# Kernel optimization log

Hardware: AMD Instinct MI355X
Metric: run time of the kernel (lower is better)

## Reference

```python
import jax, jax.numpy as jnp
import numpy as np

N, C_IN, C_OUT, T, V = 256, 64, 64, 64, 25
REL = C_IN // 8  # rel_channels = in_channels // rel_reduction (in_channels != 3)


def setup_inputs() -> dict:
    key = jax.random.key(0)
    ks = jax.random.split(key, 10)
    s_in = 1.0 / np.sqrt(C_IN)
    s_rel = 1.0 / np.sqrt(REL)
    return {
        "x": jax.random.normal(ks[0], (N, C_IN, T, V), dtype=jnp.float32),
        "A": jax.random.normal(ks[1], (V, V), dtype=jnp.float32),
        "w1": jax.random.normal(ks[2], (REL, C_IN), dtype=jnp.float32) * s_in,
        "b1": jnp.zeros((REL,), dtype=jnp.float32),
        "w2": jax.random.normal(ks[3], (REL, C_IN), dtype=jnp.float32) * s_in,
        "b2": jnp.zeros((REL,), dtype=jnp.float32),
        "w3": jax.random.normal(ks[4], (C_OUT, REL), dtype=jnp.float32) * s_rel,
        "b3": jnp.zeros((C_OUT,), dtype=jnp.float32),
        "wr": jax.random.normal(ks[5], (C_OUT, C_IN), dtype=jnp.float32) * s_in,
        "br": jnp.zeros((C_OUT,), dtype=jnp.float32),
    }


def reference(x, A, w1, b1, w2, b2, w3, b3, wr, br):
    alpha = 1.0
    # residual: 1x1 conv over channels -> (N, C_OUT, T, V)
    inputs = jnp.einsum('oi,nitv->notv', wr, x) + br[None, :, None, None]
    # conv1/conv2 then temporal mean -> (N, REL, V)
    x1 = jnp.einsum('ri,nitv->nrv', w1, x) / T + b1[None, :, None]
    x2 = jnp.einsum('ri,nitv->nrv', w2, x) / T + b2[None, :, None]
    # broadcast outer difference -> (N, REL, V, V)
    d = jnp.tanh(x1[:, :, :, None] - x2[:, :, None, :])
    # conv3 (1x1 over rel channels) -> (N, C_OUT, V, V); add static A
    Adyn = jnp.einsum('or,nruv->nouv', w3, d) + b3[None, :, None, None]
    Afull = Adyn * alpha + A[None, None, :, :]
    # per-channel batched graph conv: (N,C,V,V) x (N,C,T,V) -> (N,C,T,V)
    out = jnp.einsum('ncuv,nctv->nctu', Afull, inputs)
    return out
```

## Files before the change

### kernel.cpp

```cpp
#include <hip/hip_runtime.h>
#include <cmath>

namespace {
constexpr int NB  = 256;
constexpr int CI  = 64;
constexpr int CO  = 64;
constexpr int TT  = 64;
constexpr int V   = 25;
constexpr int REL = 8;
constexpr int TV  = TT * V;
constexpr int CC  = 8;
constexpr int IP  = 28;
constexpr int AP  = 28;
}

typedef float f4 __attribute__((ext_vector_type(4)));

__device__ __forceinline__ float fast_tanh(float x) {
  float ax = fabsf(x);
  float e  = __expf(-2.f * ax);
  float r  = (1.f - e) / (1.f + e);
  return copysignf(r, x);
}

__global__ __launch_bounds__(1024) void k1_x12(
    const float* __restrict__ x,
    const float* __restrict__ w1, const float* __restrict__ b1,
    const float* __restrict__ w2, const float* __restrict__ b2,
    float* __restrict__ ws) {
  const int n = blockIdx.x;
  const int tid = threadIdx.x;
  __shared__ __align__(16) float xs[8][TV];
  __shared__ float xsum[CI][V];
  __shared__ float w12[2][REL][CI];

  for (int idx = tid; idx < 2 * REL * CI; idx += 1024) {
    int half = idx / (REL * CI), rem = idx % (REL * CI);
    w12[half][rem / CI][rem % CI] = half ? w2[rem] : w1[rem];
  }

  const float4* xb = reinterpret_cast<const float4*>(x + (size_t)n * (CI * TV));
  float4* xsv = reinterpret_cast<float4*>(&xs[0][0]);
  constexpr int V4G = 8 * TV / 4;

  for (int g = 0; g < 8; ++g) {
    __syncthreads();
    for (int idx = tid; idx < V4G; idx += 1024)
      xsv[idx] = xb[g * V4G + idx];
    __syncthreads();
    if (tid < 8 * V) {
      int ch = tid / V, v = tid % V;
      float acc = 0.f;
      #pragma unroll
      for (int t = 0; t < TT; ++t) acc += xs[ch][t * V + v];
      xsum[g * 8 + ch][v] = acc;
    }
  }
  __syncthreads();

  if (tid < 2 * REL * V) {
    int half = tid / (REL * V), rem = tid % (REL * V);
    int r = rem / V, v = rem % V;
    float a = 0.f;
    #pragma unroll
    for (int i = 0; i < CI; ++i) a = fmaf(w12[half][r][i], xsum[i][v], a);
    ws[(size_t)n * (2 * REL * V) + tid] = a * (1.f / TT) + (half ? b2[r] : b1[r]);
  }
}

__global__ __launch_bounds__(512, 4) void k2_fused(
    const float* __restrict__ x, const float* __restrict__ A,
    const float* __restrict__ w3, const float* __restrict__ b3,
    const float* __restrict__ wr, const float* __restrict__ br,
    const float* __restrict__ ws, float* __restrict__ out) {
  const int id  = blockIdx.x;
  const int n   = (id & 7) | ((id >> 3) & ~7);
  const int cb  = (id >> 3) & 7;
  const int c0  = cb * CC;
  const int tid = threadIdx.x;

  __shared__ __align__(16) float inp[CC * TT * IP];
  __shared__ __align__(16) float Afs[CC * V * AP];

  {
    float* row = inp + tid * IP;
    row[25] = 0.f; row[26] = 0.f; row[27] = 0.f;
  }

  const float* x1n = ws + (size_t)n * (2 * REL * V);
  const float* x2n = x1n + REL * V;
  for (int idx = tid; idx < V * AP; idx += 512) {
    int u = idx / AP, v = idx % AP;
    if (v < V) {
      float t8[REL];
      #pragma unroll
      for (int r = 0; r < REL; ++r)
        t8[r] = fast_tanh(x1n[r * V + u] - x2n[r * V + v]);
      const float base = A[u * V + v];
      #pragma unroll
      for (int cc = 0; cc < CC; ++cc) {
        float acc = base + b3[c0 + cc];
        #pragma unroll
        for (int r = 0; r < REL; ++r)
          acc = fmaf(w3[(c0 + cc) * REL + r], t8[r], acc);
        Afs[(cc * V + u) * AP + v] = acc;
      }
    } else {
      #pragma unroll
      for (int cc = 0; cc < CC; ++cc)
        Afs[(cc * V + u) * AP + v] = 0.f;
    }
  }
  __syncthreads();

  if (tid < TV / 4) {
    const float* xp = x + (size_t)n * (CI * TV) + tid * 4;
    float acc[CC][4];
    #pragma unroll
    for (int cc = 0; cc < CC; ++cc) {
      float b = br[c0 + cc];
      acc[cc][0] = b; acc[cc][1] = b; acc[cc][2] = b; acc[cc][3] = b;
    }
    #pragma unroll 8
    for (int i = 0; i < CI; ++i) {
      float4 xv = *reinterpret_cast<const float4*>(xp + (size_t)i * TV);
      float w8[CC];
      #pragma unroll
      for (int cc = 0; cc < CC; ++cc)
        w8[cc] = wr[(size_t)(c0 + cc) * CI + i];
      #pragma unroll
      for (int cc = 0; cc < CC; ++cc) {
        acc[cc][0] = fmaf(w8[cc], xv.x, acc[cc][0]);
        acc[cc][1] = fmaf(w8[cc], xv.y, acc[cc][1]);
        acc[cc][2] = fmaf(w8[cc], xv.z, acc[cc][2]);
        acc[cc][3] = fmaf(w8[cc], xv.w, acc[cc][3]);
      }
    }
    int tv0 = tid * 4;
    int t = tv0 / V, v = tv0 % V;
    #pragma unroll
    for (int k = 0; k < 4; ++k) {
      #pragma unroll
      for (int cc = 0; cc < CC; ++cc)
        inp[(cc * TT + t) * IP + v] = acc[cc][k];
      if (++v == V) { v = 0; ++t; }
    }
  }
  __syncthreads();

  const int cc = tid >> 6;
  const int tq = (tid >> 2) & 15;
  const int uq = tid & 3;
  const int u0 = uq * 6;

  float acc[4][7];
  #pragma unroll
  for (int a = 0; a < 4; ++a)
    #pragma unroll
    for (int b = 0; b < 7; ++b) acc[a][b] = 0.f;

  const float* ib = &inp[(cc * TT + tq) * IP];
  const float* ab = &Afs[(cc * V + u0) * AP];

  #pragma unroll
  for (int chk = 0; chk < 7; ++chk) {
    const f4 x0 = *reinterpret_cast<const f4*>(ib + 0 * 16 * IP + chk * 4);
    const f4 x1 = *reinterpret_cast<const f4*>(ib + 1 * 16 * IP + chk * 4);
    const f4 x2 = *reinterpret_cast<const f4*>(ib + 2 * 16 * IP + chk * 4);
    const f4 x3 = *reinterpret_cast<const f4*>(ib + 3 * 16 * IP + chk * 4);
    #pragma unroll
    for (int ku = 0; ku < 7; ++ku) {
      const f4 a = *reinterpret_cast<const f4*>(ab + ku * AP + chk * 4);
      acc[0][ku] = fmaf(a.w, x0.w, fmaf(a.z, x0.z, fmaf(a.y, x0.y, fmaf(a.x, x0.x, acc[0][ku]))));
      acc[1][ku] = fmaf(a.w, x1.w, fmaf(a.z, x1.z, fmaf(a.y, x1.y, fmaf(a.x, x1.x, acc[1][ku]))));
      acc[2][ku] = fmaf(a.w, x2.w, fmaf(a.z, x2.z, fmaf(a.y, x2.y, fmaf(a.x, x2.x, acc[2][ku]))));
      acc[3][ku] = fmaf(a.w, x3.w, fmaf(a.z, x3.z, fmaf(a.y, x3.y, fmaf(a.x, x3.x, acc[3][ku]))));
    }
  }

  float* ob = out + ((size_t)n * CO + (c0 + cc)) * (size_t)(TT * V);
  #pragma unroll
  for (int ti = 0; ti < 4; ++ti) {
    const int t = tq + 16 * ti;
    #pragma unroll
    for (int ku = 0; ku < 7; ++ku)
      __builtin_nontemporal_store(acc[ti][ku], &ob[t * V + u0 + ku]);
  }
}

extern "C" void kernel_launch(void* const* d_in, const int* in_sizes, int n_in,
                              void* d_out, int out_size, void* d_ws, size_t ws_size,
                              hipStream_t stream) {
  (void)in_sizes; (void)n_in; (void)out_size; (void)ws_size;
  const float* x  = (const float*)d_in[0];
  const float* A  = (const float*)d_in[1];
  const float* w1 = (const float*)d_in[2];
  const float* b1 = (const float*)d_in[3];
  const float* w2 = (const float*)d_in[4];
  const float* b2 = (const float*)d_in[5];
  const float* w3 = (const float*)d_in[6];
  const float* b3 = (const float*)d_in[7];
  const float* wr = (const float*)d_in[8];
  const float* br = (const float*)d_in[9];
  float* out = (float*)d_out;
  float* ws  = (float*)d_ws;

  hipLaunchKernelGGL(k1_x12, dim3(NB), dim3(1024), 0, stream,
                     x, w1, b1, w2, b2, ws);
  hipLaunchKernelGGL(k2_fused, dim3(NB * CO / CC), dim3(512), 0, stream,
                     x, A, w3, b3, wr, br, ws, out);
}
```

Baseline: 143.3 us.

## Split residual and graph-conv stages into two channel halves to shrink shared memory

The fused kernel now computes the residual 1x1 conv and the graph conv in two passes of 4 channels each instead of one pass of 8. This halves the shared buffer holding the residual activations, which should allow more resident blocks per CU. The cost is extra synchronisation, x being re-read once per pass, and only half the threads doing the graph-conv work in each pass. Output stores also change from nontemporal to regular stores.

```diff
diff --git a/kernel.cpp b/kernel.cpp
--- a/kernel.cpp
+++ b/kernel.cpp
@@ -10,6 +10,7 @@
 constexpr int REL = 8;
 constexpr int TV  = TT * V;
 constexpr int CC  = 8;
+constexpr int CH  = 4;
 constexpr int IP  = 28;
 constexpr int AP  = 28;
 }
@@ -79,10 +80,10 @@
   const int c0  = cb * CC;
   const int tid = threadIdx.x;
 
-  __shared__ __align__(16) float inp[CC * TT * IP];
+  __shared__ __align__(16) float inp[CH * TT * IP];
   __shared__ __align__(16) float Afs[CC * V * AP];
 
-  {
+  if (tid < CH * TT) {
     float* row = inp + tid * IP;
     row[25] = 0.f; row[26] = 0.f; row[27] = 0.f;
   }
@@ -113,78 +114,85 @@
   }
   __syncthreads();
 
-  if (tid < TV / 4) {
-    const float* xp = x + (size_t)n * (CI * TV) + tid * 4;
-    float acc[CC][4];
-    #pragma unroll
-    for (int cc = 0; cc < CC; ++cc) {
-      float b = br[c0 + cc];
-      acc[cc][0] = b; acc[cc][1] = b; acc[cc][2] = b; acc[cc][3] = b;
-    }
-    #pragma unroll 8
-    for (int i = 0; i < CI; ++i) {
-      float4 xv = *reinterpret_cast<const float4*>(xp + (size_t)i * TV);
-      float w8[CC];
-      #pragma unroll
-      for (int cc = 0; cc < CC; ++cc)
-        w8[cc] = wr[(size_t)(c0 + cc) * CI + i];
-      #pragma unroll
-      for (int cc = 0; cc < CC; ++cc) {
-        acc[cc][0] = fmaf(w8[cc], xv.x, acc[cc][0]);
-        acc[cc][1] = fmaf(w8[cc], xv.y, acc[cc][1]);
-        acc[cc][2] = fmaf(w8[cc], xv.z, acc[cc][2]);
-        acc[cc][3] = fmaf(w8[cc], xv.w, acc[cc][3]);
-      }
-    }
-    int tv0 = tid * 4;
-    int t = tv0 / V, v = tv0 % V;
-    #pragma unroll
-    for (int k = 0; k < 4; ++k) {
-      #pragma unroll
-      for (int cc = 0; cc < CC; ++cc)
-        inp[(cc * TT + t) * IP + v] = acc[cc][k];
-      if (++v == V) { v = 0; ++t; }
-    }
-  }
-  __syncthreads();
-
-  const int cc = tid >> 6;
-  const int tq = (tid >> 2) & 15;
-  const int uq = tid & 3;
-  const int u0 = uq * 6;
-
-  float acc[4][7];
-  #pragma unroll
-  for (int a = 0; a < 4; ++a)
-    #pragma unroll
-    for (int b = 0; b < 7; ++b) acc[a][b] = 0.f;
-
-  const float* ib = &inp[(cc * TT + tq) * IP];
-  const float* ab = &Afs[(cc * V + u0) * AP];
-
-  #pragma unroll
-  for (int chk = 0; chk < 7; ++chk) {
-    const f4 x0 = *reinterpret_cast<const f4*>(ib + 0 * 16 * IP + chk * 4);
-    const f4 x1 = *reinterpret_cast<const f4*>(ib + 1 * 16 * IP + chk * 4);
-    const f4 x2 = *reinterpret_cast<const f4*>(ib + 2 * 16 * IP + chk * 4);
-    const f4 x3 = *reinterpret_cast<const f4*>(ib + 3 * 16 * IP + chk * 4);
-    #pragma unroll
-    for (int ku = 0; ku < 7; ++ku) {
-      const f4 a = *reinterpret_cast<const f4*>(ab + ku * AP + chk * 4);
-      acc[0][ku] = fmaf(a.w, x0.w, fmaf(a.z, x0.z, fmaf(a.y, x0.y, fmaf(a.x, x0.x, acc[0][ku]))));
-      acc[1][ku] = fmaf(a.w, x1.w, fmaf(a.z, x1.z, fmaf(a.y, x1.y, fmaf(a.x, x1.x, acc[1][ku]))));
-      acc[2][ku] = fmaf(a.w, x2.w, fmaf(a.z, x2.z, fmaf(a.y, x2.y, fmaf(a.x, x2.x, acc[2][ku]))));
-      acc[3][ku] = fmaf(a.w, x3.w, fmaf(a.z, x3.z, fmaf(a.y, x3.y, fmaf(a.x, x3.x, acc[3][ku]))));
-    }
-  }
-
-  float* ob = out + ((size_t)n * CO + (c0 + cc)) * (size_t)(TT * V);
-  #pragma unroll
-  for (int ti = 0; ti < 4; ++ti) {
-    const int t = tq + 16 * ti;
-    #pragma unroll
-    for (int ku = 0; ku < 7; ++ku)
-      __builtin_nontemporal_store(acc[ti][ku], &ob[t * V + u0 + ku]);
+  for (int ch = 0; ch < 2; ++ch) {
+    const int cbase = c0 + ch * CH;
+
+    if (tid < TV / 4) {
+      const float* xp = x + (size_t)n * (CI * TV) + tid * 4;
+      float acc[CH][4];
+      #pragma unroll
+      for (int cc = 0; cc < CH; ++cc) {
+        float b = br[cbase + cc];
+        acc[cc][0] = b; acc[cc][1] = b; acc[cc][2] = b; acc[cc][3] = b;
+      }
+      #pragma unroll 8
+      for (int i = 0; i < CI; ++i) {
+        float4 xv = *reinterpret_cast<const float4*>(xp + (size_t)i * TV);
+        float w4[CH];
+        #pragma unroll
+        for (int cc = 0; cc < CH; ++cc)
+          w4[cc] = wr[(size_t)(cbase + cc) * CI + i];
+        #pragma unroll
+        for (int cc = 0; cc < CH; ++cc) {
+          acc[cc][0] = fmaf(w4[cc], xv.x, acc[cc][0]);
+          acc[cc][1] = fmaf(w4[cc], xv.y, acc[cc][1]);
+          acc[cc][2] = fmaf(w4[cc], xv.z, acc[cc][2]);
+          acc[cc][3] = fmaf(w4[cc], xv.w, acc[cc][3]);
+        }
+      }
+      int tv0 = tid * 4;
+      int t = tv0 / V, v = tv0 % V;
+      #pragma unroll
+      for (int k = 0; k < 4; ++k) {
+        #pragma unroll
+        for (int cc = 0; cc < CH; ++cc)
+          inp[(cc * TT + t) * IP + v] = acc[cc][k];
+        if (++v == V) { v = 0; ++t; }
+      }
+    }
+    __syncthreads();
+
+    if (tid < 256) {
+      const int ccl = tid >> 6;
+      const int tq  = (tid >> 2) & 15;
+      const int uq  = tid & 3;
+      const int u0  = uq * 6;
+
+      float acc[4][7];
+      #pragma unroll
+      for (int a = 0; a < 4; ++a)
+        #pragma unroll
+        for (int b = 0; b < 7; ++b) acc[a][b] = 0.f;
+
+      const float* ib = &inp[(ccl * TT + tq) * IP];
+      const float* ab = &Afs[((ch * CH + ccl) * V + u0) * AP];
+
+      #pragma unroll
+      for (int chk = 0; chk < 7; ++chk) {
+        const f4 x0 = *reinterpret_cast<const f4*>(ib + 0 * 16 * IP + chk * 4);
+        const f4 x1 = *reinterpret_cast<const f4*>(ib + 1 * 16 * IP + chk * 4);
+        const f4 x2 = *reinterpret_cast<const f4*>(ib + 2 * 16 * IP + chk * 4);
+        const f4 x3 = *reinterpret_cast<const f4*>(ib + 3 * 16 * IP + chk * 4);
+        #pragma unroll
+        for (int ku = 0; ku < 7; ++ku) {
+          const f4 a = *reinterpret_cast<const f4*>(ab + ku * AP + chk * 4);
+          acc[0][ku] = fmaf(a.w, x0.w, fmaf(a.z, x0.z, fmaf(a.y, x0.y, fmaf(a.x, x0.x, acc[0][ku]))));
+          acc[1][ku] = fmaf(a.w, x1.w, fmaf(a.z, x1.z, fmaf(a.y, x1.y, fmaf(a.x, x1.x, acc[1][ku]))));
+          acc[2][ku] = fmaf(a.w, x2.w, fmaf(a.z, x2.z, fmaf(a.y, x2.y, fmaf(a.x, x2.x, acc[2][ku]))));
+          acc[3][ku] = fmaf(a.w, x3.w, fmaf(a.z, x3.z, fmaf(a.y, x3.y, fmaf(a.x, x3.x, acc[3][ku]))));
+        }
+      }
+
+      float* ob = out + ((size_t)n * CO + (cbase + ccl)) * (size_t)(TT * V);
+      #pragma unroll
+      for (int ti = 0; ti < 4; ++ti) {
+        const int t = tq + 16 * ti;
+        #pragma unroll
+        for (int ku = 0; ku < 7; ++ku)
+          ob[t * V + u0 + ku] = acc[ti][ku];
+      }
+    }
+    if (ch == 0) __syncthreads();
   }
 }
 
```

New measurement: 138.3 us (median of 2 runs). 3.5% less time.
